# Optimization experiments

Measured on AMD Instinct MI355X. Metric: run time of the kernel, lower is better.

Reference implementation:

```python
import jax, jax.numpy as jnp
import numpy as np

ROOT = 512   # size of root group
FAN = 7      # children per root node
C = ROOT * (1 + FAN)  # 4096 total nodes
MAX_DEPTH = 8  # upper bound on parent-chain length (tree depth is 2 here)


def _build_tree():
    group_offsets = [0]
    group_sizes = [ROOT]
    cid_groups = [0] * ROOT
    parents = [-1] * ROOT
    off = ROOT
    for r in range(ROOT):
        group_offsets.append(off)
        group_sizes.append(FAN)
        cid_groups += [r + 1] * FAN
        parents += [r] * FAN
        off += FAN
    return (np.asarray(group_offsets, np.int32), np.asarray(group_sizes, np.int32),
            np.asarray(cid_groups, np.int32), np.asarray(parents, np.int32))


def setup_inputs() -> dict:
    key = jax.random.key(0)
    k1, k2 = jax.random.split(key)
    x = jax.random.normal(k1, (16, C, 26, 26), dtype=jnp.float32)
    label = jax.random.randint(k2, (16, 26, 26), 0, C, dtype=jnp.int32)
    go, gs, cg, pa = _build_tree()
    return {
        "x": x,
        "label": label,
        "group_offsets": jnp.asarray(go),
        "group_sizes": jnp.asarray(gs),
        "cid_groups": jnp.asarray(cg),
        "parents": jnp.asarray(pa),
    }


def reference(x, label, group_offsets, group_sizes, cid_groups, parents):
    # x: [N, C, H, W], label: [N, H, W] with node ids in [0, C)
    N, Cn, H, W = x.shape
    G = group_offsets.shape[0]
    M = N * H * W
    xT = x.transpose(1, 0, 2, 3).reshape(Cn, M)  # [C, M], positions ordered (N,H,W)
    # segmented (per-group) stable softmax over the node axis
    gmax = jax.ops.segment_max(xT, cid_groups, num_segments=G)        # [G, M]
    shifted = xT - gmax[cid_groups]                                   # [C, M]
    e = jnp.exp(shifted)
    gsum = jax.ops.segment_sum(e, cid_groups, num_segments=G)         # [G, M]
    logp = shifted - jnp.log(gsum)[cid_groups]                        # log prob, [C, M]
    # hierarchical loss: walk parent chain from the labeled node to the root
    lab = label.reshape(M)
    cols = jnp.arange(M)
    cur = lab
    loss = jnp.zeros((), x.dtype)
    for _ in range(MAX_DEPTH):
        valid = cur >= 0
        idx = jnp.clip(cur, 0, Cn - 1)
        lp = logp[idx, cols]
        loss = loss - jnp.sum(jnp.where(valid, lp, jnp.zeros((), x.dtype)))
        cur = jnp.where(valid, parents[idx], -1)
    # BATCH_SIZE normalization (valid_normalization=False): divide by outer num N
    norm = jnp.asarray(N, x.dtype)
    loss_weight = 1.0
    return loss / norm * loss_weight
```

## Files before the change

kernel.cpp:

```cpp
#include <hip/hip_runtime.h>
#include <hip/hip_bf16.h>

#define NIMG   16
#define CTOT   4096
#define HW     676
#define MTOT   (NIMG*HW)
#define ROOTN  512
#define PPB    64
#define NBLK   (MTOT/PPB)
#define CH_PER_WAVE (ROOTN/4)

__global__ __launch_bounds__(256) void tree_loss_main(
    const float* __restrict__ x,
    const int*   __restrict__ label,
    const int*   __restrict__ group_offsets,
    const int*   __restrict__ group_sizes,
    const int*   __restrict__ cid_groups,
    const int*   __restrict__ parents,
    float*       __restrict__ ws)
{
    __shared__ float red[4][64];

    const int tid  = threadIdx.x;
    const int lane = tid & 63;
    const int wave = tid >> 6;

    const int m = blockIdx.x * PPB + lane;
    const int n = m / HW;
    const float* xb = x + (m + n * (HW * (CTOT - 1)));

    const int c0 = wave * CH_PER_WAVE;
    float a0 = 0.f, a1 = 0.f, a2 = 0.f, a3 = 0.f;
    #pragma unroll 8
    for (int cc = 0; cc < CH_PER_WAVE; cc += 4) {
        float v0 = xb[(c0 + cc + 0) * HW];
        float v1 = xb[(c0 + cc + 1) * HW];
        float v2 = xb[(c0 + cc + 2) * HW];
        float v3 = xb[(c0 + cc + 3) * HW];
        a0 += __expf(v0);
        a1 += __expf(v1);
        a2 += __expf(v2);
        a3 += __expf(v3);
    }
    red[wave][lane] = (a0 + a1) + (a2 + a3);
    __syncthreads();

    if (wave == 0) {
        float rsum = (red[0][lane] + red[1][lane]) + (red[2][lane] + red[3][lane]);

        const int lab = label[m];
        const int g   = cid_groups[lab];

        float loss_m = 0.f;
        int troot = lab;
        if (g != 0) {
            const int off = group_offsets[g];
            const int sz  = group_sizes[g];
            float csum = 0.f;
            float xlab = 0.f;
            for (int j = 0; j < sz; ++j) {
                float v = xb[(off + j) * HW];
                csum += __expf(v);
                if (off + j == lab) xlab = v;
            }
            loss_m += xlab - __logf(csum);
            troot = parents[lab];
        }
        loss_m += xb[troot * HW] - __logf(rsum);

        #pragma unroll
        for (int d = 32; d > 0; d >>= 1)
            loss_m += __shfl_down(loss_m, d, 64);
        if (lane == 0) ws[blockIdx.x] = loss_m;
    }
}

__global__ __launch_bounds__(256) void tree_loss_final(
    const float* __restrict__ ws, float* __restrict__ out)
{
    __shared__ float sm[256];
    const int t = threadIdx.x;
    float v = 0.f;
    for (int i = t; i < NBLK; i += 256) v += ws[i];
    sm[t] = v;
    __syncthreads();
    #pragma unroll
    for (int s = 128; s > 0; s >>= 1) {
        if (t < s) sm[t] += sm[t + s];
        __syncthreads();
    }
    if (t == 0) out[0] = -sm[0] * (1.0f / (float)NIMG);
}

extern "C" void kernel_launch(void* const* d_in, const int* in_sizes, int n_in,
                              void* d_out, int out_size, void* d_ws, size_t ws_size,
                              hipStream_t stream)
{
    const float* x             = (const float*)d_in[0];
    const int*   label         = (const int*)d_in[1];
    const int*   group_offsets = (const int*)d_in[2];
    const int*   group_sizes   = (const int*)d_in[3];
    const int*   cid_groups    = (const int*)d_in[4];
    const int*   parents       = (const int*)d_in[5];
    float*       out           = (float*)d_out;
    float*       ws            = (float*)d_ws;

    tree_loss_main<<<NBLK, 256, 0, stream>>>(x, label, group_offsets, group_sizes,
                                             cid_groups, parents, ws);
    tree_loss_final<<<1, 256, 0, stream>>>(ws, out);
}
```

Before: 225.7 us.

## Split root-group exp-sum across channel slices into separate kernel

The root-group exp-sum is split into four channel slices, each computed by its own block, and the partial sums are written to workspace. A new per-position kernel then combines the partials and computes the child-group and root log-probabilities. The aim is to launch four times more blocks for the bandwidth-bound root reduction so the GPU has more work in flight. The cost is an extra kernel launch plus a round trip of the partial sums through global memory.

```diff
diff --git a/kernel.cpp b/kernel.cpp
--- a/kernel.cpp
+++ b/kernel.cpp
@@ -6,11 +6,47 @@
 #define HW     676
 #define MTOT   (NIMG*HW)
 #define ROOTN  512
+#define NSLICE 4
+#define CH_PER_SLICE (ROOTN/NSLICE)
+#define CH_PER_WAVE  (CH_PER_SLICE/4)
 #define PPB    64
-#define NBLK   (MTOT/PPB)
-#define CH_PER_WAVE (ROOTN/4)
+#define NPB    (MTOT/PPB)
+#define WS_BLK (NSLICE*MTOT)
 
-__global__ __launch_bounds__(256) void tree_loss_main(
+__global__ __launch_bounds__(256) void tree_root_partial(
+    const float* __restrict__ x, float* __restrict__ ws)
+{
+    __shared__ float red[4][64];
+    const int lane = threadIdx.x & 63;
+    const int wave = threadIdx.x >> 6;
+    const int s    = blockIdx.x & 3;
+    const int pb   = blockIdx.x >> 2;
+    const int m    = pb * PPB + lane;
+    const int n    = m / HW;
+    const float* xb = x + (size_t)m + (size_t)n * (HW * (CTOT - 1));
+
+    const int c0 = s * CH_PER_SLICE + wave * CH_PER_WAVE;
+    float a0 = 0.f, a1 = 0.f, a2 = 0.f, a3 = 0.f;
+    #pragma unroll
+    for (int cc = 0; cc < CH_PER_WAVE; cc += 4) {
+        float v0 = xb[(size_t)(c0 + cc + 0) * HW];
+        float v1 = xb[(size_t)(c0 + cc + 1) * HW];
+        float v2 = xb[(size_t)(c0 + cc + 2) * HW];
+        float v3 = xb[(size_t)(c0 + cc + 3) * HW];
+        a0 += __expf(v0);
+        a1 += __expf(v1);
+        a2 += __expf(v2);
+        a3 += __expf(v3);
+    }
+    red[wave][lane] = (a0 + a1) + (a2 + a3);
+    __syncthreads();
+    if (wave == 0) {
+        float r = (red[0][lane] + red[1][lane]) + (red[2][lane] + red[3][lane]);
+        ws[s * MTOT + m] = r;
+    }
+}
+
+__global__ __launch_bounds__(64) void tree_loss_pos(
     const float* __restrict__ x,
     const int*   __restrict__ label,
     const int*   __restrict__ group_offsets,
@@ -19,60 +55,39 @@
     const int*   __restrict__ parents,
     float*       __restrict__ ws)
 {
-    __shared__ float red[4][64];
+    const int lane = threadIdx.x;
+    const int m    = blockIdx.x * PPB + lane;
+    const int n    = m / HW;
+    const float* xb = x + (size_t)m + (size_t)n * (HW * (CTOT - 1));
 
-    const int tid  = threadIdx.x;
-    const int lane = tid & 63;
-    const int wave = tid >> 6;
+    const float p0 = ws[0 * MTOT + m];
+    const float p1 = ws[1 * MTOT + m];
+    const float p2 = ws[2 * MTOT + m];
+    const float p3 = ws[3 * MTOT + m];
+    const int lab = label[m];
+    const int g   = cid_groups[lab];
 
-    const int m = blockIdx.x * PPB + lane;
-    const int n = m / HW;
-    const float* xb = x + (m + n * (HW * (CTOT - 1)));
+    float loss = 0.f;
+    int troot = lab;
+    if (g != 0) {
+        const int off = group_offsets[g];
+        const int sz  = group_sizes[g];
+        float csum = 0.f, xlab = 0.f;
+        for (int j = 0; j < sz; ++j) {
+            float v = xb[(size_t)(off + j) * HW];
+            csum += __expf(v);
+            if (off + j == lab) xlab = v;
+        }
+        loss += xlab - __logf(csum);
+        troot = parents[lab];
+    }
+    const float rsum = (p0 + p1) + (p2 + p3);
+    loss += xb[(size_t)troot * HW] - __logf(rsum);
 
-    const int c0 = wave * CH_PER_WAVE;
-    float a0 = 0.f, a1 = 0.f, a2 = 0.f, a3 = 0.f;
-    #pragma unroll 8
-    for (int cc = 0; cc < CH_PER_WAVE; cc += 4) {
-        float v0 = xb[(c0 + cc + 0) * HW];
-        float v1 = xb[(c0 + cc + 1) * HW];
-        float v2 = xb[(c0 + cc + 2) * HW];
-        float v3 = xb[(c0 + cc + 3) * HW];
-        a0 += __expf(v0);
-        a1 += __expf(v1);
-        a2 += __expf(v2);
-        a3 += __expf(v3);
-    }
-    red[wave][lane] = (a0 + a1) + (a2 + a3);
-    __syncthreads();
-
-    if (wave == 0) {
-        float rsum = (red[0][lane] + red[1][lane]) + (red[2][lane] + red[3][lane]);
-
-        const int lab = label[m];
-        const int g   = cid_groups[lab];
-
-        float loss_m = 0.f;
-        int troot = lab;
-        if (g != 0) {
-            const int off = group_offsets[g];
-            const int sz  = group_sizes[g];
-            float csum = 0.f;
-            float xlab = 0.f;
-            for (int j = 0; j < sz; ++j) {
-                float v = xb[(off + j) * HW];
-                csum += __expf(v);
-                if (off + j == lab) xlab = v;
-            }
-            loss_m += xlab - __logf(csum);
-            troot = parents[lab];
-        }
-        loss_m += xb[troot * HW] - __logf(rsum);
-
-        #pragma unroll
-        for (int d = 32; d > 0; d >>= 1)
-            loss_m += __shfl_down(loss_m, d, 64);
-        if (lane == 0) ws[blockIdx.x] = loss_m;
-    }
+    #pragma unroll
+    for (int d = 32; d > 0; d >>= 1)
+        loss += __shfl_down(loss, d, 64);
+    if (lane == 0) ws[WS_BLK + blockIdx.x] = loss;
 }
 
 __global__ __launch_bounds__(256) void tree_loss_final(
@@ -81,7 +96,7 @@
     __shared__ float sm[256];
     const int t = threadIdx.x;
     float v = 0.f;
-    for (int i = t; i < NBLK; i += 256) v += ws[i];
+    for (int i = t; i < NPB; i += 256) v += ws[WS_BLK + i];
     sm[t] = v;
     __syncthreads();
     #pragma unroll
@@ -105,7 +120,8 @@
     float*       out           = (float*)d_out;
     float*       ws            = (float*)d_ws;
 
-    tree_loss_main<<<NBLK, 256, 0, stream>>>(x, label, group_offsets, group_sizes,
-                                             cid_groups, parents, ws);
+    tree_root_partial<<<NSLICE * NPB, 256, 0, stream>>>(x, ws);
+    tree_loss_pos<<<NPB, 64, 0, stream>>>(x, label, group_offsets, group_sizes,
+                                          cid_groups, parents, ws);
     tree_loss_final<<<1, 256, 0, stream>>>(ws, out);
 }
```

Measured after the change: 225.3 us. Within noise of the previous version (-0.2%).
